# Performance work log

Hardware: AMD Instinct MI355X
Metric: run time of the kernel (lower is better)

The kernel has to match this reference:

```python
import jax, jax.numpy as jnp
import numpy as np

N, E, F_IN, F_E = 50000, 800000, 128, 16
R, H, C = 4, 4, 32            # num_relations, heads, out_channels
HC = H * C                     # 128
NEG_SLOPE = 0.2                # PyG RGATConv default negative_slope
EPS = 1e-16                    # PyG softmax epsilon


def rgat_conv(x, src, dst, edge_type, edge_attr, w, q, k, e, le, b, concat):
    """Faithful PyG RGATConv (additive-self-attention, across-relation, dim=1, aggr=add).
    x: [N,F]; w: [R,F,H*C]; q,k,e: [H*C,H]; le: [F_e,H*C]; b: bias."""
    n = x.shape[0]
    xw = jnp.einsum('nf,rfo->rno', x, w)              # [R,N,H*C] per-relation projections
    x_i = xw[edge_type, dst]                          # [E,H*C] target-node proj per edge
    x_j = xw[edge_type, src]                          # [E,H*C] source-node proj per edge
    qi = x_i @ q                                      # [E,H]
    kj = x_j @ k + (edge_attr @ le) @ e               # [E,H] (edge features folded into keys)
    alpha = jax.nn.leaky_relu(qi + kj, NEG_SLOPE)     # [E,H]
    # softmax over incoming edges of each destination node (across relations)
    amax = jax.ops.segment_max(alpha, dst, num_segments=n)
    ex = jnp.exp(alpha - amax[dst])
    denom = jax.ops.segment_sum(ex, dst, num_segments=n)
    alpha = ex / (denom[dst] + EPS)
    msg = alpha[:, :, None] * x_j.reshape(-1, H, C)   # [E,H,C]
    out = jax.ops.segment_sum(msg, dst, num_segments=n)  # [N,H,C] sum aggregation
    out = out.reshape(n, H * C) if concat else out.mean(axis=1)
    return out + b


def setup_inputs() -> dict:
    key = jax.random.key(0)
    ks = jax.random.split(key, 18)
    p = 0.05
    inp = {
        'x': jax.random.normal(ks[0], (N, F_IN), dtype=jnp.float32),
        'edge_index': jax.random.randint(ks[1], (2, E), 0, N, dtype=jnp.int64)
            if jax.config.jax_enable_x64 else jax.random.randint(ks[1], (2, E), 0, N).astype(jnp.int32),
        'edge_attr': jax.random.normal(ks[2], (E, F_E), dtype=jnp.float32),
        'edge_type': jax.random.randint(ks[3], (E,), 0, R).astype(jnp.int32),
        # conv1 params (in=F_IN, concat=True -> bias of size H*C)
        'w1': jax.random.normal(ks[4], (R, F_IN, HC), dtype=jnp.float32) * p,
        'q1': jax.random.normal(ks[5], (HC, H), dtype=jnp.float32) * p,
        'k1': jax.random.normal(ks[6], (HC, H), dtype=jnp.float32) * p,
        'e1': jax.random.normal(ks[7], (HC, H), dtype=jnp.float32) * p,
        'le1': jax.random.normal(ks[8], (F_E, HC), dtype=jnp.float32) * p,
        'b1': jnp.zeros((HC,), dtype=jnp.float32),
        # conv3 params (in=H*C=128, concat=False -> bias of size C)
        'w3': jax.random.normal(ks[9], (R, HC, HC), dtype=jnp.float32) * p,
        'q3': jax.random.normal(ks[10], (HC, H), dtype=jnp.float32) * p,
        'k3': jax.random.normal(ks[11], (HC, H), dtype=jnp.float32) * p,
        'e3': jax.random.normal(ks[12], (HC, H), dtype=jnp.float32) * p,
        'le3': jax.random.normal(ks[13], (F_E, HC), dtype=jnp.float32) * p,
        'b3': jnp.zeros((C,), dtype=jnp.float32),
    }
    return inp


def reference(x, edge_index, edge_attr, edge_type,
              w1, q1, k1, e1, le1, b1,
              w3, q3, k3, e3, le3, b3):
    src, dst = edge_index[0], edge_index[1]
    h = jax.nn.relu(rgat_conv(x, src, dst, edge_type, edge_attr,
                              w1, q1, k1, e1, le1, b1, concat=True))
    out = rgat_conv(h, src, dst, edge_type, edge_attr,
                    w3, q3, k3, e3, le3, b3, concat=False)
    return out
```

## Files before the change

kernel.cpp:

```cpp
#include <hip/hip_runtime.h>


#define NEG_SLOPE 0.2f
#define SOFT_EPS 1e-16f

typedef __attribute__((ext_vector_type(8))) short bf16x8;
typedef __attribute__((ext_vector_type(4))) float f32x4;
typedef __attribute__((ext_vector_type(4))) unsigned short u16x4;
typedef __attribute__((ext_vector_type(4))) _Float16 half4;
typedef __attribute__((ext_vector_type(8))) _Float16 half8;

__device__ __forceinline__ void bf16split(float f, unsigned short& h, unsigned short& l) {
  unsigned u = __float_as_uint(f);
  unsigned r = u + 0x7FFFu + ((u >> 16) & 1u);
  h = (unsigned short)(r >> 16);
  float fh = __uint_as_float(((unsigned)h) << 16);
  float d = f - fh;
  unsigned u2 = __float_as_uint(d);
  unsigned r2 = u2 + 0x7FFFu + ((u2 >> 16) & 1u);
  l = (unsigned short)(r2 >> 16);
}


__device__ __forceinline__ void hist_body(int id, const int* __restrict__ dst,
                                          int* __restrict__ deg, int E) {
  int e = id * 256 + (int)threadIdx.x;
  if (e < E) atomicAdd(&deg[dst[e]], 1);
}

__device__ __forceinline__ void convx_body(int id, const float* __restrict__ in,
                                           unsigned short* __restrict__ hi,
                                           unsigned short* __restrict__ lo, int total8) {
  int i = id * 256 + (int)threadIdx.x;
  if (i >= total8) return;
  const float4* p = (const float4*)in + (size_t)i * 2;
  float4 a = p[0], b = p[1];
  float v[8] = {a.x, a.y, a.z, a.w, b.x, b.y, b.z, b.w};
  bf16x8 hv, lv;
#pragma unroll
  for (int j = 0; j < 8; ++j) {
    unsigned short h, l;
    bf16split(v[j], h, l);
    hv[j] = (short)h; lv[j] = (short)l;
  }
  *(bf16x8*)(hi + (size_t)i * 8) = hv;
  *(bf16x8*)(lo + (size_t)i * 8) = lv;
}

__device__ __forceinline__ void convw_body(int idx, const float* __restrict__ w1,
                                           const float* __restrict__ w3,
                                           unsigned short* __restrict__ wF1h,
                                           unsigned short* __restrict__ wF1l,
                                           unsigned short* __restrict__ wF3h,
                                           unsigned short* __restrict__ wF3l) {
  if (idx >= 131072) return;
  int L = idx >> 16;
  int rem = idx & 65535;
  int r = rem >> 14, rem2 = rem & 16383, f = rem2 >> 7, o = rem2 & 127;
  const float* w = L ? w3 : w1;
  unsigned short* dh = L ? wF3h : wF1h;
  unsigned short* dl = L ? wF3l : wF1l;
  float v = w[(r * 128 + f) * 128 + o];
  unsigned short h, l;
  bf16split(v, h, l);
  int ot = o >> 4, c = o & 15, kc = f >> 5, q = (f >> 3) & 3, j = f & 7;
  int di = r * 16384 + ((((ot * 4 + kc) * 4 + q) * 16 + c) * 8 + j);
  dh[di] = h;
  dl[di] = l;
}

__device__ __forceinline__ void wqk_body(int idx, const float* __restrict__ w1,
                                         const float* __restrict__ q1, const float* __restrict__ k1,
                                         const float* __restrict__ w3, const float* __restrict__ q3,
                                         const float* __restrict__ k3, float* __restrict__ wqk) {
  if (idx >= 8192) return;
  int L = idx >> 12, rem = idx & 4095;
  int r = rem >> 10, rem2 = rem & 1023, f = rem2 >> 3, j = rem2 & 7;
  const float* w = L ? w3 : w1;
  const float* qk = (j < 4) ? (L ? q3 : q1) : (L ? k3 : k1);
  int h = j & 3;
  const float* wrow = w + (r * 128 + f) * 128;
  float acc = 0.f;
  for (int o = 0; o < 128; ++o) acc += wrow[o] * qk[o * 4 + h];
  wqk[idx] = acc;
}

__device__ __forceinline__ void lee_body(const float* __restrict__ le1, const float* __restrict__ e1,
                                         const float* __restrict__ le3, const float* __restrict__ e3,
                                         float* __restrict__ lee) {
  int t = threadIdx.x;
  if (t >= 128) return;
  const float* le = (t < 64) ? le1 : le3;
  const float* ee = (t < 64) ? e1 : e3;
  int u = t & 63, f = u >> 2, h = u & 3;
  float acc = 0.f;
  for (int o = 0; o < 128; ++o) acc += le[f * 128 + o] * ee[o * 4 + h];
  lee[t] = acc;
}

__global__ __launch_bounds__(256) void pre_kernel(
    const int* __restrict__ dst, int* __restrict__ deg, int E,
    const float* __restrict__ x, unsigned short* __restrict__ xhi,
    unsigned short* __restrict__ xlo, int total8,
    const float* __restrict__ w1, const float* __restrict__ q1, const float* __restrict__ k1,
    const float* __restrict__ w3, const float* __restrict__ q3, const float* __restrict__ k3,
    float* __restrict__ wqk,
    const float* __restrict__ le1, const float* __restrict__ e1,
    const float* __restrict__ le3, const float* __restrict__ e3, float* __restrict__ lee,
    unsigned short* __restrict__ wF1h, unsigned short* __restrict__ wF1l,
    unsigned short* __restrict__ wF3h, unsigned short* __restrict__ wF3l,
    int nAB, int eb, int cxb) {
  int bid = blockIdx.x;
  if (bid < nAB) {
    int id = bid >> 1;
    if (bid & 1) {
      if (id < eb) hist_body(id, dst, deg, E);
    } else {
      if (id < cxb) convx_body(id, x, xhi, xlo, total8);
    }
  } else {
    int b2 = bid - nAB;
    if (b2 < 512) {
      convw_body(b2 * 256 + (int)threadIdx.x, w1, w3, wF1h, wF1l, wF3h, wF3l);
    } else if (b2 < 544) {
      wqk_body((b2 - 512) * 256 + (int)threadIdx.x, w1, q1, k1, w3, q3, k3, wqk);
    } else {
      lee_body(le1, e1, le3, e3, lee);
    }
  }
}


__global__ __launch_bounds__(256) void scanA_kernel(const int* __restrict__ deg,
                                                    int* __restrict__ bsum, int N) {
  int b = blockIdx.x, t = threadIdx.x;
  int base = b * 1024 + t * 4;
  int s = 0;
#pragma unroll
  for (int j = 0; j < 4; ++j) {
    int i = base + j;
    if (i < N) s += deg[i];
  }
#pragma unroll
  for (int o = 1; o < 64; o <<= 1) s += __shfl_xor(s, o);
  __shared__ int wsum[4];
  if ((t & 63) == 0) wsum[t >> 6] = s;
  __syncthreads();
  if (t == 0) bsum[b] = wsum[0] + wsum[1] + wsum[2] + wsum[3];
}

__global__ __launch_bounds__(256) void scanB_kernel(const int* __restrict__ bsum,
                                                    int* __restrict__ boff,
                                                    int* __restrict__ row_start,
                                                    int nb, int N) {
  int t = threadIdx.x;
  int v = (t < nb) ? bsum[t] : 0;
  int inc = v;
#pragma unroll
  for (int o = 1; o < 64; o <<= 1) {
    int u = __shfl_up(inc, o);
    if ((t & 63) >= o) inc += u;
  }
  __shared__ int wt[4];
  if ((t & 63) == 63) wt[t >> 6] = inc;
  __syncthreads();
  int add = 0;
  for (int wv = 0; wv < (t >> 6); ++wv) add += wt[wv];
  inc += add;
  if (t < nb) boff[t] = inc - v;
  if (t == 255) row_start[N] = inc;
}

__global__ __launch_bounds__(256) void scanC_kernel(const int* __restrict__ deg,
                                                    const int* __restrict__ boff,
                                                    int* __restrict__ row_start,
                                                    int* __restrict__ cursor, int N) {
  int b = blockIdx.x, t = threadIdx.x;
  int base = b * 1024 + t * 4;
  int d[4];
  int s = 0;
#pragma unroll
  for (int j = 0; j < 4; ++j) {
    int i = base + j;
    d[j] = (i < N) ? deg[i] : 0;
    s += d[j];
  }
  int inc = s;
#pragma unroll
  for (int o = 1; o < 64; o <<= 1) {
    int u = __shfl_up(inc, o);
    if ((t & 63) >= o) inc += u;
  }
  __shared__ int wt[4];
  if ((t & 63) == 63) wt[t >> 6] = inc;
  __syncthreads();
  int add = boff[b];
  for (int wv = 0; wv < (t >> 6); ++wv) add += wt[wv];
  int off = add + inc - s;
#pragma unroll
  for (int j = 0; j < 4; ++j) {
    int i = base + j;
    if (i < N) {
      row_start[i] = off;
      cursor[i] = off;
      off += d[j];
    }
  }
}


__device__ __forceinline__ void scatter_body(int id, const int* __restrict__ src,
                                             const int* __restrict__ dst,
                                             const int* __restrict__ et,
                                             int* __restrict__ cursor,
                                             int4* __restrict__ es, int E) {
  int e = id * 256 + (int)threadIdx.x;
  if (e >= E) return;
  int d = dst[e];
  int pos = atomicAdd(&cursor[d], 1);
  es[pos] = make_int4(src[e], d, et[e], e);
}

__device__ __forceinline__ void qkx_body(int nbid, char* smem, const float* __restrict__ xin,
                                         const float* __restrict__ wqk, float* __restrict__ qn,
                                         float* __restrict__ kn, int N) {
  float* swqk = (float*)smem;
  int t = threadIdx.x;
#pragma unroll
  for (int j = 0; j < 16; ++j) {
    int i = j * 256 + t;
    swqk[(i >> 10) * 1032 + (i & 1023)] = wqk[i];
  }
  __syncthreads();
  int nb = nbid * 64;
  int rl = t >> 2, r = t & 3;
  int n = nb + rl;
  int nc = n < N ? n : N - 1;
  const float4* xr = (const float4*)(xin + (size_t)nc * 128);
  const float* wb = swqk + r * 1032;
  float aq0 = 0, aq1 = 0, aq2 = 0, aq3 = 0;
  float ak0 = 0, ak1 = 0, ak2 = 0, ak3 = 0;
#pragma unroll 4
  for (int f4 = 0; f4 < 32; ++f4) {
    float4 xv = xr[f4];
    const float* w0 = wb + f4 * 32;
    float4 qa = *(const float4*)(w0);
    float4 ka = *(const float4*)(w0 + 4);
    float4 qb = *(const float4*)(w0 + 8);
    float4 kb = *(const float4*)(w0 + 12);
    float4 qc = *(const float4*)(w0 + 16);
    float4 kc = *(const float4*)(w0 + 20);
    float4 qd = *(const float4*)(w0 + 24);
    float4 kd = *(const float4*)(w0 + 28);
    aq0 += xv.x * qa.x + xv.y * qb.x + xv.z * qc.x + xv.w * qd.x;
    aq1 += xv.x * qa.y + xv.y * qb.y + xv.z * qc.y + xv.w * qd.y;
    aq2 += xv.x * qa.z + xv.y * qb.z + xv.z * qc.z + xv.w * qd.z;
    aq3 += xv.x * qa.w + xv.y * qb.w + xv.z * qc.w + xv.w * qd.w;
    ak0 += xv.x * ka.x + xv.y * kb.x + xv.z * kc.x + xv.w * kd.x;
    ak1 += xv.x * ka.y + xv.y * kb.y + xv.z * kc.y + xv.w * kd.y;
    ak2 += xv.x * ka.z + xv.y * kb.z + xv.z * kc.z + xv.w * kd.z;
    ak3 += xv.x * ka.w + xv.y * kb.w + xv.z * kc.w + xv.w * kd.w;
  }
  if (n < N) {
    *(float4*)(qn + ((size_t)r * N + n) * 4) = make_float4(aq0, aq1, aq2, aq3);
    *(float4*)(kn + ((size_t)r * N + n) * 4) = make_float4(ak0, ak1, ak2, ak3);
  }
}

__global__ __launch_bounds__(256) void sc_kernel(
    const int* __restrict__ src, const int* __restrict__ dst, const int* __restrict__ et,
    int* __restrict__ cursor, int4* __restrict__ es, int E,
    const float* __restrict__ xin, const float* __restrict__ wqk,
    float* __restrict__ qn, float* __restrict__ kn, int N, int qxb) {
  extern __shared__ char smem[];
  int bid = blockIdx.x;
  int g = bid / 5, r5 = bid - g * 5;
  if (r5 == 4) {
    if (g < qxb) qkx_body(g, smem, xin, wqk, qn, kn, N);
  } else {
    scatter_body(g * 4 + r5, src, dst, et, cursor, es, E);
  }
}


__device__ __forceinline__ void ek2_body(int id, char* smem, const int4* __restrict__ es,
                                         const float* __restrict__ ea,
                                         const float* __restrict__ lee,
                                         float* __restrict__ eks1, float* __restrict__ eks3,
                                         int E) {
  float* sl = (float*)smem;
  if (threadIdx.x < 128) sl[threadIdx.x] = lee[threadIdx.x];
  __syncthreads();
  int i = id * 256 + (int)threadIdx.x;
  if (i >= E) return;
  int eid = es[i].w;
  const float4* a4 = (const float4*)(ea + (size_t)eid * 16);
  float a1[4] = {0, 0, 0, 0}, a3[4] = {0, 0, 0, 0};
#pragma unroll
  for (int ii = 0; ii < 4; ++ii) {
    float4 v = a4[ii];
    int f = ii * 4;
#pragma unroll
    for (int h = 0; h < 4; ++h) {
      a1[h] += v.x * sl[f * 4 + h] + v.y * sl[(f + 1) * 4 + h] +
               v.z * sl[(f + 2) * 4 + h] + v.w * sl[(f + 3) * 4 + h];
      a3[h] += v.x * sl[64 + f * 4 + h] + v.y * sl[64 + (f + 1) * 4 + h] +
               v.z * sl[64 + (f + 2) * 4 + h] + v.w * sl[64 + (f + 3) * 4 + h];
    }
  }
  *(float4*)(eks1 + (size_t)i * 4) = make_float4(a1[0], a1[1], a1[2], a1[3]);
  *(float4*)(eks3 + (size_t)i * 4) = make_float4(a3[0], a3[1], a3[2], a3[3]);
}

__device__ __forceinline__ void proj_body(int pid,
                                          const unsigned short* __restrict__ xhi,
                                          const unsigned short* __restrict__ xlo,
                                          const unsigned short* __restrict__ wFh,
                                          const unsigned short* __restrict__ wFl,
                                          _Float16* __restrict__ xwh, int N) {
  int r = pid & 3;
  int nb = (pid >> 2) * 128;
  int t = threadIdx.x;
  int wv = t >> 6;
  int lane = t & 63;
  int c = lane & 15, q = lane >> 4;
  const bf16x8* whp = (const bf16x8*)(wFh + r * 16384) + lane;
  const bf16x8* wlp = (const bf16x8*)(wFl + r * 16384) + lane;
  int nodebase = nb + wv * 32;
  int n0 = nodebase + c;
  int n1 = nodebase + 16 + c;
  int n0c = n0 < N ? n0 : N - 1;
  int n1c = n1 < N ? n1 : N - 1;

  f32x4 acc[8][2];
#pragma unroll
  for (int ot = 0; ot < 8; ++ot)
#pragma unroll
    for (int nt = 0; nt < 2; ++nt) acc[ot][nt] = (f32x4){0.f, 0.f, 0.f, 0.f};

  bf16x8 xb[2][4];
  {
    int k0 = q * 8;
    xb[0][0] = *(const bf16x8*)(xhi + (size_t)n0c * 128 + k0);
    xb[0][1] = *(const bf16x8*)(xlo + (size_t)n0c * 128 + k0);
    xb[0][2] = *(const bf16x8*)(xhi + (size_t)n1c * 128 + k0);
    xb[0][3] = *(const bf16x8*)(xlo + (size_t)n1c * 128 + k0);
  }
#pragma unroll
  for (int kc = 0; kc < 4; ++kc) {
    if (kc < 3) {
      int k0 = (kc + 1) * 32 + q * 8;
      xb[(kc + 1) & 1][0] = *(const bf16x8*)(xhi + (size_t)n0c * 128 + k0);
      xb[(kc + 1) & 1][1] = *(const bf16x8*)(xlo + (size_t)n0c * 128 + k0);
      xb[(kc + 1) & 1][2] = *(const bf16x8*)(xhi + (size_t)n1c * 128 + k0);
      xb[(kc + 1) & 1][3] = *(const bf16x8*)(xlo + (size_t)n1c * 128 + k0);
    }
    bf16x8 b0h = xb[kc & 1][0], b0l = xb[kc & 1][1];
    bf16x8 b1h = xb[kc & 1][2], b1l = xb[kc & 1][3];
#pragma unroll
    for (int ot = 0; ot < 8; ++ot) {
      bf16x8 ah = whp[(ot * 4 + kc) * 64];
      bf16x8 al = wlp[(ot * 4 + kc) * 64];
      acc[ot][0] = __builtin_amdgcn_mfma_f32_16x16x32_bf16(ah, b0h, acc[ot][0], 0, 0, 0);
      acc[ot][0] = __builtin_amdgcn_mfma_f32_16x16x32_bf16(ah, b0l, acc[ot][0], 0, 0, 0);
      acc[ot][0] = __builtin_amdgcn_mfma_f32_16x16x32_bf16(al, b0h, acc[ot][0], 0, 0, 0);
      acc[ot][1] = __builtin_amdgcn_mfma_f32_16x16x32_bf16(ah, b1h, acc[ot][1], 0, 0, 0);
      acc[ot][1] = __builtin_amdgcn_mfma_f32_16x16x32_bf16(ah, b1l, acc[ot][1], 0, 0, 0);
      acc[ot][1] = __builtin_amdgcn_mfma_f32_16x16x32_bf16(al, b1h, acc[ot][1], 0, 0, 0);
    }
  }

#pragma unroll
  for (int nt = 0; nt < 2; ++nt) {
    int n = nodebase + nt * 16 + c;
    if (n < N) {
      _Float16* basep = xwh + ((size_t)r * N + n) * 128 + q * 4;
#pragma unroll
      for (int ot = 0; ot < 8; ++ot) {
        f32x4 a = acc[ot][nt];
        half4 hv;
        hv[0] = (_Float16)a.x; hv[1] = (_Float16)a.y;
        hv[2] = (_Float16)a.z; hv[3] = (_Float16)a.w;
        *(half4*)(basep + ot * 16) = hv;
      }
    }
  }
}

__global__ __launch_bounds__(256) void ep1_kernel(
    const int4* __restrict__ es, const float* __restrict__ ea, const float* __restrict__ lee,
    float* __restrict__ eks1, float* __restrict__ eks3, int E,
    const unsigned short* __restrict__ xhi, const unsigned short* __restrict__ xlo,
    const unsigned short* __restrict__ wFh, const unsigned short* __restrict__ wFl,
    _Float16* __restrict__ xwh, int N, int pjb) {
  extern __shared__ char smem[];
  int bid = blockIdx.x;
  int g = bid / 3, r3 = bid - g * 3;
  if (r3 == 2) {
    if (g < pjb) proj_body(g, xhi, xlo, wFh, wFl, xwh, N);
  } else {
    ek2_body(g * 2 + r3, smem, es, ea, lee, eks1, eks3, E);
  }
}

__global__ __launch_bounds__(256) void p2_kernel(
    const unsigned short* __restrict__ xhi, const unsigned short* __restrict__ xlo,
    const unsigned short* __restrict__ wFh, const unsigned short* __restrict__ wFl,
    _Float16* __restrict__ xwh, int N,
    const float* __restrict__ xin, const float* __restrict__ wqk,
    float* __restrict__ qn, float* __restrict__ kn, int pjb, int qxb) {
  extern __shared__ char smem[];
  int bid = blockIdx.x;
  int g = bid / 3, r3 = bid - g * 3;
  if (r3 == 2) {
    if (g < qxb) qkx_body(g, smem, xin, wqk, qn, kn, N);
  } else {
    int id = g * 2 + r3;
    if (id < pjb) proj_body(id, xhi, xlo, wFh, wFl, xwh, N);
  }
}


__device__ __forceinline__ float4 edge_alpha(const int4* __restrict__ es,
                                             const float* __restrict__ qn,
                                             const float* __restrict__ kn,
                                             const float* __restrict__ eks,
                                             int i, int d, int N) {
  int4 v = es[i];
  float4 kv = *(const float4*)(kn + (v.z * N + v.x) * 4);
  float4 ev = ((const float4*)eks)[i];
  float4 q4 = *(const float4*)(qn + (v.z * N + d) * 4);
  float4 a = make_float4(q4.x + kv.x + ev.x, q4.y + kv.y + ev.y,
                         q4.z + kv.z + ev.z, q4.w + kv.w + ev.w);
  a.x = a.x > 0.f ? a.x : NEG_SLOPE * a.x;
  a.y = a.y > 0.f ? a.y : NEG_SLOPE * a.y;
  a.z = a.z > 0.f ? a.z : NEG_SLOPE * a.z;
  a.w = a.w > 0.f ? a.w : NEG_SLOPE * a.w;
  return a;
}

__device__ __forceinline__ float4 max4(float4 a, float4 b) {
  return make_float4(fmaxf(a.x, b.x), fmaxf(a.y, b.y), fmaxf(a.z, b.z), fmaxf(a.w, b.w));
}

__global__ __launch_bounds__(256) void agg_kernel(
    const int4* __restrict__ es, const int* __restrict__ row_start,
    const float* __restrict__ qn, const float* __restrict__ kn,
    const float* __restrict__ eks, float* __restrict__ alpha_s,
    const _Float16* __restrict__ xwh, const float* __restrict__ bias,
    float* __restrict__ out, unsigned short* __restrict__ xhi,
    unsigned short* __restrict__ xlo, int N, int concat) {
  int d = blockIdx.x * 16 + (threadIdx.x >> 4);
  if (d >= N) return;
  int ql = threadIdx.x & 15;
  int rs = row_start[d], re = row_start[d + 1];
  int deg = re - rs;
  int h = ql >> 2;

  float acc[8];
#pragma unroll
  for (int j = 0; j < 8; ++j) acc[j] = 0.f;
  float rden = 0.f;

  if (deg > 0) {
    float4 m = make_float4(-1e30f, -1e30f, -1e30f, -1e30f);
    float4 ar0 = m, ar1 = m, ar2 = m, ar3 = m;
    bool fast = (deg <= 64);
    bool v0 = ql < deg, v1 = 16 + ql < deg, v2 = 32 + ql < deg, v3 = 48 + ql < deg;
    if (fast) {
      int dm1 = deg - 1;
      int o0 = v0 ? ql : dm1;
      int o1 = v1 ? 16 + ql : dm1;
      int o2 = v2 ? 32 + ql : dm1;
      int o3 = v3 ? 48 + ql : dm1;
      float4 a0 = edge_alpha(es, qn, kn, eks, rs + o0, d, N);
      float4 a1 = edge_alpha(es, qn, kn, eks, rs + o1, d, N);
      float4 a2 = edge_alpha(es, qn, kn, eks, rs + o2, d, N);
      float4 a3 = edge_alpha(es, qn, kn, eks, rs + o3, d, N);
      if (v0) { ar0 = a0; m = max4(m, a0); }
      if (v1) { ar1 = a1; m = max4(m, a1); }
      if (v2) { ar2 = a2; m = max4(m, a2); }
      if (v3) { ar3 = a3; m = max4(m, a3); }
    } else {
      for (int i = rs + ql; i < re; i += 16) {
        float4 a = edge_alpha(es, qn, kn, eks, i, d, N);
        ((float4*)alpha_s)[i] = a;
        m = max4(m, a);
      }
    }
#pragma unroll
    for (int o = 1; o < 16; o <<= 1) {
      m.x = fmaxf(m.x, __shfl_xor(m.x, o));
      m.y = fmaxf(m.y, __shfl_xor(m.y, o));
      m.z = fmaxf(m.z, __shfl_xor(m.z, o));
      m.w = fmaxf(m.w, __shfl_xor(m.w, o));
    }

    float4 s = make_float4(0.f, 0.f, 0.f, 0.f);
    if (fast) {
#define SWEEPB(V, AR, OFF)                                                   \
      if (V) {                                                               \
        float4 e4 = make_float4(__expf(AR.x - m.x), __expf(AR.y - m.y),      \
                                __expf(AR.z - m.z), __expf(AR.w - m.w));     \
        ((float4*)alpha_s)[rs + OFF + ql] = e4;                              \
        s.x += e4.x; s.y += e4.y; s.z += e4.z; s.w += e4.w;                  \
      }
      SWEEPB(v0, ar0, 0)
      SWEEPB(v1, ar1, 16)
      SWEEPB(v2, ar2, 32)
      SWEEPB(v3, ar3, 48)
#undef SWEEPB
    } else {
      for (int i = rs + ql; i < re; i += 16) {
        float4 a = ((const float4*)alpha_s)[i];
        float4 e4 = make_float4(__expf(a.x - m.x), __expf(a.y - m.y),
                                __expf(a.z - m.z), __expf(a.w - m.w));
        ((float4*)alpha_s)[i] = e4;
        s.x += e4.x; s.y += e4.y; s.z += e4.z; s.w += e4.w;
      }
    }
#pragma unroll
    for (int o = 1; o < 16; o <<= 1) {
      s.x += __shfl_xor(s.x, o); s.y += __shfl_xor(s.y, o);
      s.z += __shfl_xor(s.z, o); s.w += __shfl_xor(s.w, o);
    }
    float smh = (h == 0) ? s.x : (h == 1) ? s.y : (h == 2) ? s.z : s.w;
    rden = 1.f / (smh + SOFT_EPS);

    int e = rs;
    for (; e + 4 <= re; e += 4) {
      int4 a0 = es[e];
      int4 a1 = es[e + 1];
      int4 a2 = es[e + 2];
      int4 a3 = es[e + 3];
      float w0 = alpha_s[e * 4 + h];
      float w1 = alpha_s[(e + 1) * 4 + h];
      float w2 = alpha_s[(e + 2) * 4 + h];
      float w3 = alpha_s[(e + 3) * 4 + h];
      half8 x0 = *(const half8*)(xwh + (a0.z * N + a0.x) * 128 + ql * 8);
      half8 x1 = *(const half8*)(xwh + (a1.z * N + a1.x) * 128 + ql * 8);
      half8 x2 = *(const half8*)(xwh + (a2.z * N + a2.x) * 128 + ql * 8);
      half8 x3 = *(const half8*)(xwh + (a3.z * N + a3.x) * 128 + ql * 8);
#pragma unroll
      for (int j = 0; j < 8; ++j) {
        acc[j] = fmaf((float)x0[j], w0, acc[j]);
        acc[j] = fmaf((float)x1[j], w1, acc[j]);
        acc[j] = fmaf((float)x2[j], w2, acc[j]);
        acc[j] = fmaf((float)x3[j], w3, acc[j]);
      }
    }
    for (; e < re; ++e) {
      int4 a0 = es[e];
      float w0 = alpha_s[e * 4 + h];
      half8 x0 = *(const half8*)(xwh + (a0.z * N + a0.x) * 128 + ql * 8);
#pragma unroll
      for (int j = 0; j < 8; ++j) acc[j] = fmaf((float)x0[j], w0, acc[j]);
    }
  }
#pragma unroll
  for (int j = 0; j < 8; ++j) acc[j] *= rden;

  if (concat) {
    float4 b0 = ((const float4*)bias)[ql * 2];
    float4 b1 = ((const float4*)bias)[ql * 2 + 1];
    float v[8] = {acc[0] + b0.x, acc[1] + b0.y, acc[2] + b0.z, acc[3] + b0.w,
                  acc[4] + b1.x, acc[5] + b1.y, acc[6] + b1.z, acc[7] + b1.w};
    u16x4 hv0, lv0, hv1, lv1;
#pragma unroll
    for (int j = 0; j < 8; ++j) {
      v[j] = v[j] > 0.f ? v[j] : 0.f;
      unsigned short hh, ll;
      bf16split(v[j], hh, ll);
      if (j < 4) { hv0[j] = hh; lv0[j] = ll; }
      else { hv1[j - 4] = hh; lv1[j - 4] = ll; }
    }
    float* orow = out + (size_t)d * 128 + ql * 8;
    *(float4*)orow = make_float4(v[0], v[1], v[2], v[3]);
    *(float4*)(orow + 4) = make_float4(v[4], v[5], v[6], v[7]);
    *(u16x4*)(xhi + (size_t)d * 128 + ql * 8) = hv0;
    *(u16x4*)(xhi + (size_t)d * 128 + ql * 8 + 4) = hv1;
    *(u16x4*)(xlo + (size_t)d * 128 + ql * 8) = lv0;
    *(u16x4*)(xlo + (size_t)d * 128 + ql * 8 + 4) = lv1;
  } else {
#pragma unroll
    for (int j = 0; j < 8; ++j) {
      acc[j] += __shfl_xor(acc[j], 4);
      acc[j] += __shfl_xor(acc[j], 8);
    }
    if (ql < 4) {
      float4 b0 = ((const float4*)bias)[ql * 2];
      float4 b1 = ((const float4*)bias)[ql * 2 + 1];
      float* orow = out + (size_t)d * 32 + ql * 8;
      *(float4*)orow = make_float4(0.25f * acc[0] + b0.x, 0.25f * acc[1] + b0.y,
                                   0.25f * acc[2] + b0.z, 0.25f * acc[3] + b0.w);
      *(float4*)(orow + 4) = make_float4(0.25f * acc[4] + b1.x, 0.25f * acc[5] + b1.y,
                                         0.25f * acc[6] + b1.z, 0.25f * acc[7] + b1.w);
    }
  }
}

extern "C" void kernel_launch(void* const* d_in, const int* in_sizes, int n_in,
                              void* d_out, int out_size, void* d_ws, size_t ws_size,
                              hipStream_t stream) {
  const float* x   = (const float*)d_in[0];
  const int*   ei  = (const int*)d_in[1];
  const float* ea  = (const float*)d_in[2];
  const int*   etp = (const int*)d_in[3];
  const float* w1  = (const float*)d_in[4];
  const float* q1  = (const float*)d_in[5];
  const float* k1  = (const float*)d_in[6];
  const float* e1  = (const float*)d_in[7];
  const float* le1 = (const float*)d_in[8];
  const float* b1  = (const float*)d_in[9];
  const float* w3  = (const float*)d_in[10];
  const float* q3  = (const float*)d_in[11];
  const float* k3  = (const float*)d_in[12];
  const float* e3  = (const float*)d_in[13];
  const float* le3 = (const float*)d_in[14];
  const float* b3  = (const float*)d_in[15];
  const int N = in_sizes[0] / 128;
  const int E = in_sizes[3];
  const int* srcp = ei;
  const int* dstp = ei + E;

  float* ws   = (float*)d_ws;
  _Float16* xwh = (_Float16*)ws;
  float* qn   = ws + (size_t)2 * N * 128;
  float* kn   = qn + (size_t)4 * N * 4;
  float* eks1 = kn + (size_t)4 * N * 4;
  float* eks3 = eks1 + (size_t)E * 4;
  float* alph = eks3 + (size_t)E * 4;
  float* hbuf = alph + (size_t)E * 4;
  float* leeb = hbuf + (size_t)N * 128;
  float* wqkb = leeb + 128;
  int* deg      = (int*)(wqkb + 8192);
  int* rowst    = deg + N;
  int* cursor   = rowst + N + 1;
  int* bsum     = cursor + N;
  int* boff     = bsum + 256;
  uintptr_t pe = (uintptr_t)(boff + 256);
  pe = (pe + 15) & ~(uintptr_t)15;
  int4* es      = (int4*)pe;
  uintptr_t pa = (uintptr_t)(es + E);
  pa = (pa + 255) & ~(uintptr_t)255;
  unsigned short* xhi  = (unsigned short*)pa;
  unsigned short* xlo  = xhi + (size_t)N * 128;
  unsigned short* wF1h = xlo + (size_t)N * 128;
  unsigned short* wF1l = wF1h + 4 * 128 * 128;
  unsigned short* wF3h = wF1l + 4 * 128 * 128;
  unsigned short* wF3l = wF3h + 4 * 128 * 128;
  (void)ws_size; (void)n_in; (void)out_size;

  int eb   = (E + 255) / 256;
  int nb16 = (N + 15) / 16;
  int nbs  = (N + 1023) / 1024;
  int pgy  = (N + 127) / 128;
  int pjb  = 4 * pgy;
  int qxb  = (N + 63) / 64;
  int cxb  = (N * 128 / 8 + 255) / 256;

  hipMemsetAsync(deg, 0, (size_t)N * sizeof(int), stream);

  int M = eb > cxb ? eb : cxb;
  int nAB = 2 * M;
  int preg = nAB + 512 + 32 + 1;
  pre_kernel<<<preg, 256, 0, stream>>>(dstp, deg, E, x, xhi, xlo, N * 128 / 8,
                                       w1, q1, k1, w3, q3, k3, wqkb,
                                       le1, e1, le3, e3, leeb,
                                       wF1h, wF1l, wF3h, wF3l, nAB, eb, cxb);
  scanA_kernel<<<nbs, 256, 0, stream>>>(deg, bsum, N);
  scanB_kernel<<<1, 256, 0, stream>>>(bsum, boff, rowst, nbs, N);
  scanC_kernel<<<nbs, 256, 0, stream>>>(deg, boff, rowst, cursor, N);

  int scq = (eb + 3) / 4;
  int scg = 5 * (scq > qxb ? scq : qxb);
  sc_kernel<<<scg, 256, 16512, stream>>>(srcp, dstp, etp, cursor, es, E,
                                         x, wqkb, qn, kn, N, qxb);

  int ekh = (eb + 1) / 2;
  int e1g = 3 * (ekh > pjb ? ekh : pjb);
  ep1_kernel<<<e1g, 256, 512, stream>>>(es, ea, leeb, eks1, eks3, E,
                                        xhi, xlo, wF1h, wF1l, xwh, N, pjb);

  agg_kernel<<<nb16, 256, 0, stream>>>(es, rowst, qn, kn, eks1, alph, xwh,
                                       b1, hbuf, xhi, xlo, N, 1);

  int pjh = (pjb + 1) / 2;
  int p2g = 3 * (pjh > qxb ? pjh : qxb);
  p2_kernel<<<p2g, 256, 16512, stream>>>(xhi, xlo, wF3h, wF3l, xwh, N,
                                         hbuf, wqkb + 4096, qn, kn, pjb, qxb);

  agg_kernel<<<nb16, 256, 0, stream>>>(es, rowst, qn, kn, eks3, alph, xwh,
                                       b3, (float*)d_out, xhi, xlo, N, 0);
}
```

Before: 479.3 us.

## Stage projection weights in LDS and split output columns across blocks

The projection body now copies half of the per-relation bf16 hi/lo weight matrix (64 output columns) into 32 KB of shared memory and reads MFMA A-operands from LDS instead of global memory. Each block covers half the output width, so the projection block count doubles and the accumulator array is halved, which lowers register pressure. The fused ep1 and p2 launches are rebalanced to match the new projection block counts. The cost is an extra LDS fill and barrier per block, twice the x-tile loads, and 32 KB of dynamic shared memory per block, which may limit occupancy.

After: 443.2 us. 1.08x faster.

```diff
diff --git a/kernel.cpp b/kernel.cpp
--- a/kernel.cpp
+++ b/kernel.cpp
@@ -312,29 +312,40 @@
   *(float4*)(eks3 + (size_t)i * 4) = make_float4(a3[0], a3[1], a3[2], a3[3]);
 }
 
-__device__ __forceinline__ void proj_body(int pid,
+__device__ __forceinline__ void proj_body(int pid, char* smem,
                                           const unsigned short* __restrict__ xhi,
                                           const unsigned short* __restrict__ xlo,
                                           const unsigned short* __restrict__ wFh,
                                           const unsigned short* __restrict__ wFl,
                                           _Float16* __restrict__ xwh, int N) {
+  bf16x8* wl_h = (bf16x8*)smem;
+  bf16x8* wl_l = wl_h + 1024;
   int r = pid & 3;
-  int nb = (pid >> 2) * 128;
+  int h0 = (pid >> 2) & 1;
+  int nb = (pid >> 3) * 128;
   int t = threadIdx.x;
+  const bf16x8* srcH = (const bf16x8*)(wFh + r * 16384) + h0 * 1024;
+  const bf16x8* srcL = (const bf16x8*)(wFl + r * 16384) + h0 * 1024;
+#pragma unroll
+  for (int j = 0; j < 4; ++j) {
+    int i = j * 256 + t;
+    wl_h[i] = srcH[i];
+    wl_l[i] = srcL[i];
+  }
+  __syncthreads();
+
   int wv = t >> 6;
   int lane = t & 63;
   int c = lane & 15, q = lane >> 4;
-  const bf16x8* whp = (const bf16x8*)(wFh + r * 16384) + lane;
-  const bf16x8* wlp = (const bf16x8*)(wFl + r * 16384) + lane;
   int nodebase = nb + wv * 32;
   int n0 = nodebase + c;
   int n1 = nodebase + 16 + c;
   int n0c = n0 < N ? n0 : N - 1;
   int n1c = n1 < N ? n1 : N - 1;
 
-  f32x4 acc[8][2];
-#pragma unroll
-  for (int ot = 0; ot < 8; ++ot)
+  f32x4 acc[4][2];
+#pragma unroll
+  for (int ot = 0; ot < 4; ++ot)
 #pragma unroll
     for (int nt = 0; nt < 2; ++nt) acc[ot][nt] = (f32x4){0.f, 0.f, 0.f, 0.f};
 
@@ -358,9 +369,10 @@
     bf16x8 b0h = xb[kc & 1][0], b0l = xb[kc & 1][1];
     bf16x8 b1h = xb[kc & 1][2], b1l = xb[kc & 1][3];
 #pragma unroll
-    for (int ot = 0; ot < 8; ++ot) {
-      bf16x8 ah = whp[(ot * 4 + kc) * 64];
-      bf16x8 al = wlp[(ot * 4 + kc) * 64];
+    for (int ot = 0; ot < 4; ++ot) {
+      int fi = ((ot * 4 + kc) * 4 + q) * 16 + c;
+      bf16x8 ah = wl_h[fi];
+      bf16x8 al = wl_l[fi];
       acc[ot][0] = __builtin_amdgcn_mfma_f32_16x16x32_bf16(ah, b0h, acc[ot][0], 0, 0, 0);
       acc[ot][0] = __builtin_amdgcn_mfma_f32_16x16x32_bf16(ah, b0l, acc[ot][0], 0, 0, 0);
       acc[ot][0] = __builtin_amdgcn_mfma_f32_16x16x32_bf16(al, b0h, acc[ot][0], 0, 0, 0);
@@ -374,9 +386,9 @@
   for (int nt = 0; nt < 2; ++nt) {
     int n = nodebase + nt * 16 + c;
     if (n < N) {
-      _Float16* basep = xwh + ((size_t)r * N + n) * 128 + q * 4;
-#pragma unroll
-      for (int ot = 0; ot < 8; ++ot) {
+      _Float16* basep = xwh + ((size_t)r * N + n) * 128 + h0 * 64 + q * 4;
+#pragma unroll
+      for (int ot = 0; ot < 4; ++ot) {
         f32x4 a = acc[ot][nt];
         half4 hv;
         hv[0] = (_Float16)a.x; hv[1] = (_Float16)a.y;
@@ -392,14 +404,15 @@
     float* __restrict__ eks1, float* __restrict__ eks3, int E,
     const unsigned short* __restrict__ xhi, const unsigned short* __restrict__ xlo,
     const unsigned short* __restrict__ wFh, const unsigned short* __restrict__ wFl,
-    _Float16* __restrict__ xwh, int N, int pjb) {
+    _Float16* __restrict__ xwh, int N, int eb, int pjb) {
   extern __shared__ char smem[];
   int bid = blockIdx.x;
   int g = bid / 3, r3 = bid - g * 3;
-  if (r3 == 2) {
-    if (g < pjb) proj_body(g, xhi, xlo, wFh, wFl, xwh, N);
+  if (r3 == 0) {
+    if (g < eb) ek2_body(g, smem, es, ea, lee, eks1, eks3, E);
   } else {
-    ek2_body(g * 2 + r3, smem, es, ea, lee, eks1, eks3, E);
+    int id = g * 2 + (r3 - 1);
+    if (id < pjb) proj_body(id, smem, xhi, xlo, wFh, wFl, xwh, N);
   }
 }
 
@@ -411,12 +424,12 @@
     float* __restrict__ qn, float* __restrict__ kn, int pjb, int qxb) {
   extern __shared__ char smem[];
   int bid = blockIdx.x;
-  int g = bid / 3, r3 = bid - g * 3;
-  if (r3 == 2) {
+  int g = bid / 5, r5 = bid - g * 5;
+  if (r5 == 4) {
     if (g < qxb) qkx_body(g, smem, xin, wqk, qn, kn, N);
   } else {
-    int id = g * 2 + r3;
-    if (id < pjb) proj_body(id, xhi, xlo, wFh, wFl, xwh, N);
+    int id = g * 4 + r5;
+    if (id < pjb) proj_body(id, smem, xhi, xlo, wFh, wFl, xwh, N);
   }
 }
 
@@ -655,7 +668,7 @@
   int nb16 = (N + 15) / 16;
   int nbs  = (N + 1023) / 1024;
   int pgy  = (N + 127) / 128;
-  int pjb  = 4 * pgy;
+  int pjb  = 8 * pgy;
   int qxb  = (N + 63) / 64;
   int cxb  = (N * 128 / 8 + 255) / 256;
 
@@ -677,18 +690,18 @@
   sc_kernel<<<scg, 256, 16512, stream>>>(srcp, dstp, etp, cursor, es, E,
                                          x, wqkb, qn, kn, N, qxb);
 
-  int ekh = (eb + 1) / 2;
-  int e1g = 3 * (ekh > pjb ? ekh : pjb);
-  ep1_kernel<<<e1g, 256, 512, stream>>>(es, ea, leeb, eks1, eks3, E,
-                                        xhi, xlo, wF1h, wF1l, xwh, N, pjb);
+  int pjh = (pjb + 1) / 2;
+  int e1grp = eb > pjh ? eb : pjh;
+  ep1_kernel<<<3 * e1grp, 256, 32768, stream>>>(es, ea, leeb, eks1, eks3, E,
+                                                xhi, xlo, wF1h, wF1l, xwh, N, eb, pjb);
 
   agg_kernel<<<nb16, 256, 0, stream>>>(es, rowst, qn, kn, eks1, alph, xwh,
                                        b1, hbuf, xhi, xlo, N, 1);
 
-  int pjh = (pjb + 1) / 2;
-  int p2g = 3 * (pjh > qxb ? pjh : qxb);
-  p2_kernel<<<p2g, 256, 16512, stream>>>(xhi, xlo, wF3h, wF3l, xwh, N,
-                                         hbuf, wqkb + 4096, qn, kn, pjb, qxb);
+  int pjq = (pjb + 3) / 4;
+  int p2grp = pjq > qxb ? pjq : qxb;
+  p2_kernel<<<5 * p2grp, 256, 32768, stream>>>(xhi, xlo, wF3h, wF3l, xwh, N,
+                                               hbuf, wqkb + 4096, qn, kn, pjb, qxb);
 
   agg_kernel<<<nb16, 256, 0, stream>>>(es, rowst, qn, kn, eks3, alph, xwh,
                                        b3, (float*)d_out, xhi, xlo, N, 0);
```
